# Performance work log

Hardware: AMD Instinct MI355X
Metric: run time of the kernel (lower is better)

Reference implementation:

```python
import jax, jax.numpy as jnp
import numpy as np

ALPHA = 0.25
GAMMA = 2.0
W_CLASS = 2.0
W_BBOX = 5.0
W_GIOU = 2.0
EPS = 1e-8

BS, Q, NUM_CLASSES, M_PER_IMG = 16, 900, 80, 100


def box_cxcywh_to_xyxy(b):
    cx, cy, w, h = jnp.split(b, 4, axis=-1)
    return jnp.concatenate([cx - 0.5 * w, cy - 0.5 * h, cx + 0.5 * w, cy + 0.5 * h], axis=-1)


def box_xyxy_to_cxcywh(b):
    x1, y1, x2, y2 = jnp.split(b, 4, axis=-1)
    return jnp.concatenate([(x1 + x2) * 0.5, (y1 + y2) * 0.5, x2 - x1, y2 - y1], axis=-1)


def generalized_box_iou(a, b):
    # a: [N,4], b: [M,4], xyxy -> [N,M] GIoU
    area_a = (a[:, 2] - a[:, 0]) * (a[:, 3] - a[:, 1])
    area_b = (b[:, 2] - b[:, 0]) * (b[:, 3] - b[:, 1])
    lt = jnp.maximum(a[:, None, :2], b[None, :, :2])
    rb = jnp.minimum(a[:, None, 2:], b[None, :, 2:])
    wh = jnp.clip(rb - lt, 0.0)
    inter = wh[..., 0] * wh[..., 1]
    union = area_a[:, None] + area_b[None, :] - inter
    iou = inter / union
    lt_c = jnp.minimum(a[:, None, :2], b[None, :, :2])
    rb_c = jnp.maximum(a[:, None, 2:], b[None, :, 2:])
    wh_c = jnp.clip(rb_c - lt_c, 0.0)
    area_c = wh_c[..., 0] * wh_c[..., 1]
    return iou - (area_c - union) / area_c


def setup_inputs() -> dict:
    key = jax.random.key(0)
    k1, k2, k3, k4 = jax.random.split(key, 4)
    pred_logits = jax.random.normal(k1, (BS, Q, NUM_CLASSES), dtype=jnp.float32)
    pred_boxes = jax.random.uniform(k2, (BS, Q, 4), dtype=jnp.float32)  # cxcywh in (0,1)
    T = BS * M_PER_IMG
    tgt_cxcywh = jax.random.uniform(k3, (T, 4), dtype=jnp.float32)
    # keep widths/heights in a sane positive range, produce valid xyxy
    tgt_cxcywh = tgt_cxcywh.at[:, 2:].set(0.05 + 0.5 * tgt_cxcywh[:, 2:])
    tgt_boxes = box_cxcywh_to_xyxy(tgt_cxcywh)
    tgt_labels = jax.random.randint(k4, (T,), 0, NUM_CLASSES, dtype=jnp.int64)
    return {"pred_logits": pred_logits, "pred_boxes": pred_boxes,
            "tgt_boxes": tgt_boxes, "tgt_labels": tgt_labels}


def reference(pred_logits, pred_boxes, tgt_boxes, tgt_labels):
    bs, q, _ = pred_logits.shape
    out_prob = jax.nn.sigmoid(pred_logits.reshape(bs * q, -1))  # [NQ, C]
    out_bbox = pred_boxes.reshape(bs * q, 4)                    # [NQ, 4] cxcywh
    # focal-style classification cost
    neg_cost = (1.0 - ALPHA) * out_prob ** GAMMA * (-jnp.log(1.0 - out_prob + EPS))
    pos_cost = ALPHA * (1.0 - out_prob) ** GAMMA * (-jnp.log(out_prob + EPS))
    cost_class = (pos_cost - neg_cost)[:, tgt_labels]           # [NQ, T]
    # L1 cost in cxcywh space
    tgt_cxcywh = box_xyxy_to_cxcywh(tgt_boxes)
    cost_bbox = jnp.sum(jnp.abs(out_bbox[:, None, :] - tgt_cxcywh[None, :, :]), axis=-1)
    # GIoU cost in xyxy space
    cost_giou = -generalized_box_iou(box_cxcywh_to_xyxy(out_bbox), tgt_boxes)
    C = W_BBOX * cost_bbox + W_CLASS * cost_class + W_GIOU * cost_giou
    return C.reshape(bs, q, -1)  # [bs, Q, T_total]; per-image block i is C[i, :, i*M:(i+1)*M]
```

## Files before the change

kernel.cpp:

```cpp
#include <hip/hip_runtime.h>
#include <math.h>


#define NCLS  80
#define QTILE 4
#define NTHR  256

typedef float v2f __attribute__((ext_vector_type(2)));

static __device__ __forceinline__ v2f v2(float a, float b) { v2f r; r.x = a; r.y = b; return r; }
static __device__ __forceinline__ v2f vmax2(v2f a, v2f b) { return v2(fmaxf(a.x, b.x), fmaxf(a.y, b.y)); }
static __device__ __forceinline__ v2f vmin2(v2f a, v2f b) { return v2(fminf(a.x, b.x), fminf(a.y, b.y)); }

__global__ __launch_bounds__(NTHR)
void matcher_cost_kernel(const float* __restrict__ logits,
                         const float* __restrict__ pboxes,
                         const float* __restrict__ tboxes,
                         const int*   __restrict__ tlabels,
                         float* __restrict__ out,
                         int NQ, int T)
{
    __shared__ float ccT[NCLS][QTILE];

    const int tid = threadIdx.x;
    const int q0  = blockIdx.x * QTILE;

    for (int i = tid; i < QTILE * NCLS; i += NTHR) {
        int q = i / NCLS, lab = i - q * NCLS;
        float x = logits[(size_t)q0 * NCLS + i];
        float p = 1.0f / (1.0f + __expf(-x));
        float pos = 0.25f * (1.0f - p) * (1.0f - p) * (-__logf(p + 1e-8f));
        float neg = 0.75f * p * p * (-__logf(1.0f - p + 1e-8f));
        ccT[lab][q] = 2.0f * (pos - neg) + 2.0f;
    }

    float qx1[QTILE], qy1[QTILE], qx2[QTILE], qy2[QTILE];
    float qcx[QTILE], qcy[QTILE], qw[QTILE], qh[QTILE], qa[QTILE];
#pragma unroll
    for (int q = 0; q < QTILE; ++q) {
        float4 pb = reinterpret_cast<const float4*>(pboxes)[q0 + q];
        qcx[q] = pb.x; qcy[q] = pb.y; qw[q] = pb.z; qh[q] = pb.w;
        qx1[q] = pb.x - 0.5f * pb.z;  qy1[q] = pb.y - 0.5f * pb.w;
        qx2[q] = pb.x + 0.5f * pb.z;  qy2[q] = pb.y + 0.5f * pb.w;
        qa[q]  = (qx2[q] - qx1[q]) * (qy2[q] - qy1[q]);
    }
    __syncthreads();

    const float4* tb4 = reinterpret_cast<const float4*>(tboxes);
    const int2*   lb2 = reinterpret_cast<const int2*>(tlabels);
    const float4* ccv = reinterpret_cast<const float4*>(ccT);

    const int npair = T >> 1;
    float2* obase = reinterpret_cast<float2*>(out) + (size_t)q0 * npair;

    for (int pair = tid; pair < npair; pair += NTHR) {
        const int t0 = pair << 1;
        float4 b0 = tb4[t0], b1 = tb4[t0 + 1];
        int2 L = lb2[pair];
        float4 c0 = ccv[L.x], c1 = ccv[L.y];

        v2f bx1 = v2(b0.x, b1.x), by1 = v2(b0.y, b1.y);
        v2f bx2 = v2(b0.z, b1.z), by2 = v2(b0.w, b1.w);
        v2f bw  = bx2 - bx1;
        v2f bh  = by2 - by1;
        v2f bcx = 0.5f * (bx1 + bx2);
        v2f bcy = 0.5f * (by1 + by2);
        v2f ba  = bw * bh;

#pragma unroll
        for (int q = 0; q < QTILE; ++q) {
            v2f dcx = qcx[q] - bcx, dcy = qcy[q] - bcy;
            v2f dw  = qw[q]  - bw,  dh  = qh[q]  - bh;
            float l1a = (fabsf(dcx.x) + fabsf(dcy.x)) + (fabsf(dw.x) + fabsf(dh.x));
            float l1b = (fabsf(dcx.y) + fabsf(dcy.y)) + (fabsf(dw.y) + fabsf(dh.y));

            v2f ix1 = vmax2(v2(qx1[q], qx1[q]), bx1);
            v2f iy1 = vmax2(v2(qy1[q], qy1[q]), by1);
            v2f ix2 = vmin2(v2(qx2[q], qx2[q]), bx2);
            v2f iy2 = vmin2(v2(qy2[q], qy2[q]), by2);
            v2f iwd = ix2 - ix1, ihd = iy2 - iy1;
            v2f iw = vmax2(iwd, v2(0.f, 0.f));
            v2f ih = vmax2(ihd, v2(0.f, 0.f));
            v2f inter = iw * ih;
            v2f uni = (qa[q] + ba) - inter;
            v2f cw = (qw[q] + bw) - iwd;
            v2f ch = (qh[q] + bh) - ihd;
            v2f ca = cw * ch;

            float clsa = (q == 0) ? c0.x : (q == 1) ? c0.y : (q == 2) ? c0.z : c0.w;
            float clsb = (q == 0) ? c1.x : (q == 1) ? c1.y : (q == 2) ? c1.z : c1.w;

            v2f base = v2(fmaf(5.0f, l1a, clsa), fmaf(5.0f, l1b, clsb));
            v2f den  = uni * ca;
            v2f r    = v2(__builtin_amdgcn_rcpf(den.x),
                          __builtin_amdgcn_rcpf(den.y));
            v2f ica  = inter * ca;
            v2f num  = uni * uni + ica;
            v2f nr   = num * r;
            v2f res  = -2.0f * nr + base;

            obase[q * npair + pair] = make_float2(res.x, res.y);
        }
    }
}

extern "C" void kernel_launch(void* const* d_in, const int* in_sizes, int n_in,
                              void* d_out, int out_size, void* d_ws, size_t ws_size,
                              hipStream_t stream) {
    const float* logits  = (const float*)d_in[0];
    const float* pboxes  = (const float*)d_in[1];
    const float* tboxes  = (const float*)d_in[2];
    const int*   tlabels = (const int*)d_in[3];
    float* out = (float*)d_out;

    const int NQ = in_sizes[1] / 4;
    const int T  = in_sizes[2] / 4;

    const int nblocks = (NQ + QTILE - 1) / QTILE;
    matcher_cost_kernel<<<nblocks, NTHR, 0, stream>>>(logits, pboxes, tboxes,
                                                      tlabels, out, NQ, T);
}
```

Before: 31.66 us.

## Reformulate GIoU intersection via center distances and prefetch next target pair

```diff
diff --git a/kernel.cpp b/kernel.cpp
--- a/kernel.cpp
+++ b/kernel.cpp
@@ -9,8 +9,6 @@
 typedef float v2f __attribute__((ext_vector_type(2)));
 
 static __device__ __forceinline__ v2f v2(float a, float b) { v2f r; r.x = a; r.y = b; return r; }
-static __device__ __forceinline__ v2f vmax2(v2f a, v2f b) { return v2(fmaxf(a.x, b.x), fmaxf(a.y, b.y)); }
-static __device__ __forceinline__ v2f vmin2(v2f a, v2f b) { return v2(fminf(a.x, b.x), fminf(a.y, b.y)); }
 
 __global__ __launch_bounds__(NTHR)
 void matcher_cost_kernel(const float* __restrict__ logits,
@@ -34,15 +32,14 @@
         ccT[lab][q] = 2.0f * (pos - neg) + 2.0f;
     }
 
-    float qx1[QTILE], qy1[QTILE], qx2[QTILE], qy2[QTILE];
-    float qcx[QTILE], qcy[QTILE], qw[QTILE], qh[QTILE], qa[QTILE];
+    float qcx[QTILE], qcy[QTILE], qw[QTILE], qh[QTILE];
+    float qwh[QTILE], qhh[QTILE], qa[QTILE];
 #pragma unroll
     for (int q = 0; q < QTILE; ++q) {
         float4 pb = reinterpret_cast<const float4*>(pboxes)[q0 + q];
         qcx[q] = pb.x; qcy[q] = pb.y; qw[q] = pb.z; qh[q] = pb.w;
-        qx1[q] = pb.x - 0.5f * pb.z;  qy1[q] = pb.y - 0.5f * pb.w;
-        qx2[q] = pb.x + 0.5f * pb.z;  qy2[q] = pb.y + 0.5f * pb.w;
-        qa[q]  = (qx2[q] - qx1[q]) * (qy2[q] - qy1[q]);
+        qwh[q] = 0.5f * pb.z; qhh[q] = 0.5f * pb.w;
+        qa[q]  = pb.z * pb.w;
     }
     __syncthreads();
 
@@ -53,54 +50,64 @@
     const int npair = T >> 1;
     float2* obase = reinterpret_cast<float2*>(out) + (size_t)q0 * npair;
 
-    for (int pair = tid; pair < npair; pair += NTHR) {
-        const int t0 = pair << 1;
-        float4 b0 = tb4[t0], b1 = tb4[t0 + 1];
-        int2 L = lb2[pair];
+    int pair = tid;
+    float4 b0 = tb4[pair * 2], b1 = tb4[pair * 2 + 1];
+    int2 L = lb2[pair];
+
+    for (;;) {
+        const int  nxt  = pair + NTHR;
+        const bool more = nxt < npair;
+        const int  nc   = more ? nxt : pair;
+        float4 nb0 = tb4[nc * 2], nb1 = tb4[nc * 2 + 1];
+        int2   nL  = lb2[nc];
+
         float4 c0 = ccv[L.x], c1 = ccv[L.y];
 
-        v2f bx1 = v2(b0.x, b1.x), by1 = v2(b0.y, b1.y);
-        v2f bx2 = v2(b0.z, b1.z), by2 = v2(b0.w, b1.w);
-        v2f bw  = bx2 - bx1;
-        v2f bh  = by2 - by1;
-        v2f bcx = 0.5f * (bx1 + bx2);
-        v2f bcy = 0.5f * (by1 + by2);
+        v2f bX1 = v2(b0.x, b1.x), bY1 = v2(b0.y, b1.y);
+        v2f bX2 = v2(b0.z, b1.z), bY2 = v2(b0.w, b1.w);
+        v2f bw  = bX2 - bX1,      bh  = bY2 - bY1;
+        v2f bcx = 0.5f * (bX1 + bX2);
+        v2f bcy = 0.5f * (bY1 + bY2);
         v2f ba  = bw * bh;
+        v2f bwh = 0.5f * bw,      bhh = 0.5f * bh;
 
 #pragma unroll
         for (int q = 0; q < QTILE; ++q) {
             v2f dcx = qcx[q] - bcx, dcy = qcy[q] - bcy;
             v2f dw  = qw[q]  - bw,  dh  = qh[q]  - bh;
-            float l1a = (fabsf(dcx.x) + fabsf(dcy.x)) + (fabsf(dw.x) + fabsf(dh.x));
-            float l1b = (fabsf(dcx.y) + fabsf(dcy.y)) + (fabsf(dw.y) + fabsf(dh.y));
+            v2f adx = v2(fabsf(dcx.x), fabsf(dcx.y));
+            v2f ady = v2(fabsf(dcy.x), fabsf(dcy.y));
+            v2f l1  = (adx + ady) + v2(fabsf(dw.x) + fabsf(dh.x),
+                                       fabsf(dw.y) + fabsf(dh.y));
 
-            v2f ix1 = vmax2(v2(qx1[q], qx1[q]), bx1);
-            v2f iy1 = vmax2(v2(qy1[q], qy1[q]), by1);
-            v2f ix2 = vmin2(v2(qx2[q], qx2[q]), bx2);
-            v2f iy2 = vmin2(v2(qy2[q], qy2[q]), by2);
-            v2f iwd = ix2 - ix1, ihd = iy2 - iy1;
-            v2f iw = vmax2(iwd, v2(0.f, 0.f));
-            v2f ih = vmax2(ihd, v2(0.f, 0.f));
+            v2f hw  = qwh[q] + bwh,  hh  = qhh[q] + bhh;
+            v2f dwh = qwh[q] - bwh,  dhh = qhh[q] - bhh;
+            v2f ewx = v2(fmaxf(adx.x, fabsf(dwh.x)), fmaxf(adx.y, fabsf(dwh.y)));
+            v2f ewy = v2(fmaxf(ady.x, fabsf(dhh.x)), fmaxf(ady.y, fabsf(dhh.y)));
+            v2f iwd = hw - ewx,      ihd = hh - ewy;
+            v2f iw  = v2(fmaxf(iwd.x, 0.f), fmaxf(iwd.y, 0.f));
+            v2f ih  = v2(fmaxf(ihd.x, 0.f), fmaxf(ihd.y, 0.f));
             v2f inter = iw * ih;
             v2f uni = (qa[q] + ba) - inter;
-            v2f cw = (qw[q] + bw) - iwd;
-            v2f ch = (qh[q] + bh) - ihd;
+            v2f cw = 2.0f * hw - iwd;
+            v2f ch = 2.0f * hh - ihd;
             v2f ca = cw * ch;
 
             float clsa = (q == 0) ? c0.x : (q == 1) ? c0.y : (q == 2) ? c0.z : c0.w;
             float clsb = (q == 0) ? c1.x : (q == 1) ? c1.y : (q == 2) ? c1.z : c1.w;
 
-            v2f base = v2(fmaf(5.0f, l1a, clsa), fmaf(5.0f, l1b, clsb));
+            v2f base = 5.0f * l1 + v2(clsa, clsb);
             v2f den  = uni * ca;
             v2f r    = v2(__builtin_amdgcn_rcpf(den.x),
                           __builtin_amdgcn_rcpf(den.y));
-            v2f ica  = inter * ca;
-            v2f num  = uni * uni + ica;
-            v2f nr   = num * r;
-            v2f res  = -2.0f * nr + base;
+            v2f num  = uni * uni + inter * ca;
+            v2f res  = -2.0f * (num * r) + base;
 
             obase[q * npair + pair] = make_float2(res.x, res.y);
         }
+
+        if (!more) break;
+        pair = nxt; b0 = nb0; b1 = nb1; L = nL;
     }
 }
 
```

After: 31.18 us. Within noise of the previous version (-1.5%).
